# Performance work log

Hardware: AMD Instinct MI355X
Metric: run time of the kernel (lower is better)

Reference implementation:

```python
import jax, jax.numpy as jnp
import numpy as np

N, P, D, C = 2048, 64, 512, 32   # bs*n_vars, patch_num, hidden_dim, cluster_num
H, DFF, L = 8, 2048, 3           # heads, ffn dim, encoder layers
TEMP = 10.0
EPS = 1e-10
LN_EPS = 1e-5


def setup_inputs() -> dict:
    key = jax.random.key(0)
    ks = jax.random.split(key, 18)
    s = 0.02  # small init to keep activations sane
    inp = {}
    inp["input_series"] = jax.random.normal(ks[0], (N, P, D), jnp.float32)
    pi = jax.random.uniform(ks[1], (C,), jnp.float32) + 0.1
    inp["text_pi"] = pi / pi.sum()
    A = jax.random.uniform(ks[2], (C, C), jnp.float32) + 0.1
    inp["text_A"] = A / A.sum(axis=1, keepdims=True)
    # stacked per-layer TransformerEncoderLayer params (torch post-norm, relu)
    inp["qkv_w"] = jax.random.normal(ks[3], (L, 3 * D, D), jnp.float32) * s
    inp["qkv_b"] = jnp.zeros((L, 3 * D), jnp.float32)
    inp["out_w"] = jax.random.normal(ks[4], (L, D, D), jnp.float32) * s
    inp["out_b"] = jnp.zeros((L, D), jnp.float32)
    inp["ln1_w"] = jnp.ones((L, D), jnp.float32)
    inp["ln1_b"] = jnp.zeros((L, D), jnp.float32)
    inp["ff1_w"] = jax.random.normal(ks[5], (L, DFF, D), jnp.float32) * s
    inp["ff1_b"] = jnp.zeros((L, DFF), jnp.float32)
    inp["ff2_w"] = jax.random.normal(ks[6], (L, D, DFF), jnp.float32) * s
    inp["ff2_b"] = jnp.zeros((L, D), jnp.float32)
    inp["ln2_w"] = jnp.ones((L, D), jnp.float32)
    inp["ln2_b"] = jnp.zeros((L, D), jnp.float32)
    inp["mus"] = jax.random.normal(ks[7], (C, D), jnp.float32)
    return inp


def _layer_norm(x, w, b):
    m = x.mean(axis=-1, keepdims=True)
    v = ((x - m) ** 2).mean(axis=-1, keepdims=True)
    return (x - m) * jax.lax.rsqrt(v + LN_EPS) * w + b


def _encoder_layer(x, qkv_w, qkv_b, out_w, out_b, ln1_w, ln1_b,
                   ff1_w, ff1_b, ff2_w, ff2_b, ln2_w, ln2_b):
    n, p, d = x.shape
    dh = d // H
    qkv = x @ qkv_w.T + qkv_b                       # [n,p,3d]
    q, k, v = jnp.split(qkv, 3, axis=-1)
    def split_heads(t):
        return t.reshape(n, p, H, dh).transpose(0, 2, 1, 3)  # [n,h,p,dh]
    q, k, v = split_heads(q), split_heads(k), split_heads(v)
    scores = jnp.einsum('nhqd,nhkd->nhqk', q, k) / (dh ** 0.5)
    attn = jax.nn.softmax(scores, axis=-1)
    o = jnp.einsum('nhqk,nhkd->nhqd', attn, v)
    o = o.transpose(0, 2, 1, 3).reshape(n, p, d)
    o = o @ out_w.T + out_b
    x = _layer_norm(x + o, ln1_w, ln1_b)            # post-norm
    f = jax.nn.relu(x @ ff1_w.T + ff1_b) @ ff2_w.T + ff2_b
    return _layer_norm(x + f, ln2_w, ln2_b)


def reference(input_series, text_pi, text_A, qkv_w, qkv_b, out_w, out_b,
              ln1_w, ln1_b, ff1_w, ff1_b, ff2_w, ff2_b, ln2_w, ln2_b, mus):
    x = input_series
    for l in range(L):
        x = _encoder_layer(x, qkv_w[l], qkv_b[l], out_w[l], out_b[l],
                           ln1_w[l], ln1_b[l], ff1_w[l], ff1_b[l],
                           ff2_w[l], ff2_b[l], ln2_w[l], ln2_b[l])
    emb_ts = x                                       # [N,P,D]
    # ClusterCenters: softmax of exp(-||x - tanh(mu)||^2 / T)
    mu = jnp.tanh(mus)                               # [C,D]
    dist = ((emb_ts ** 2).sum(-1)[..., None]
            + (mu ** 2).sum(-1)[None, None, :]
            - 2.0 * jnp.einsum('npd,cd->npc', emb_ts, mu))  # [N,P,C]
    z = jnp.exp(-dist / TEMP)
    logits_all = z / z.sum(axis=-1, keepdims=True)
    log_za = jnp.log(logits_all + EPS)               # [N,P,C]
    # sequential HMM-style recursion over patches
    l0 = jax.nn.softmax(jnp.log(text_pi + EPS)[None, :] + log_za[:, 0], axis=-1)
    def step(c, lz):
        c2 = jax.nn.softmax(jnp.log(c @ text_A + EPS) + lz, axis=-1)
        return c2, c2
    _, ys = jax.lax.scan(step, l0, jnp.swapaxes(log_za[:, 1:], 0, 1))  # [P-1,N,C]
    cluster_probs = jnp.concatenate([l0[:, None], jnp.swapaxes(ys, 0, 1)], axis=1)
    entropy_loss = -jnp.sum(cluster_probs * jnp.log(cluster_probs + EPS), axis=-1).mean()
    return (cluster_probs, emb_ts, text_pi, text_A, entropy_loss)
```

## Files before the change

kernel.cpp:

```cpp
#include <hip/hip_runtime.h>
#include <stdint.h>


typedef __bf16 bf16;
typedef __bf16 bf16x2 __attribute__((ext_vector_type(2)));
typedef __bf16 bf16x4 __attribute__((ext_vector_type(4)));
typedef __bf16 bf16x8 __attribute__((ext_vector_type(8)));
typedef float  f32x4  __attribute__((ext_vector_type(4)));
typedef float  f32x2  __attribute__((ext_vector_type(2)));

#define EPSF 1e-10f
#define NROWS 131072L

__device__ __forceinline__ float bflo(uint32_t u){ return __uint_as_float(u << 16); }
__device__ __forceinline__ float bfhi(uint32_t u){ return __uint_as_float(u & 0xffff0000u); }

__device__ __forceinline__ void gload_lds16(const bf16* g, bf16* l){
  __builtin_amdgcn_global_load_lds((const __attribute__((address_space(1))) uint32_t*)g,
                                   (__attribute__((address_space(3))) uint32_t*)l,
                                   16, 0, 0);
}

__global__ void k_f2bf(const float* __restrict__ in, bf16* __restrict__ out, long n){
  const long stride = (long)gridDim.x * blockDim.x * 4;
  for (long i = ((long)blockIdx.x * blockDim.x + threadIdx.x) * 4; i < n; i += stride){
    f32x4 v = *(const f32x4*)(in + i);
    bf16x4 o = { (bf16)v[0], (bf16)v[1], (bf16)v[2], (bf16)v[3] };
    *(bf16x4*)(out + i) = o;
  }
}


#define MFMA_PH(RH, CH)                                                       \
  {                                                                           \
    __builtin_amdgcn_s_setprio(1);                                            \
    _Pragma("unroll")                                                         \
    for (int i2 = 0; i2 < 4; i2++) {                                          \
      _Pragma("unroll")                                                       \
      for (int j2 = 0; j2 < 2; j2++) {                                        \
        acc[(RH)*4+i2][(CH)*2+j2] = __builtin_amdgcn_mfma_f32_16x16x32_bf16(  \
            a[i2][0], b[CH][j2][0], acc[(RH)*4+i2][(CH)*2+j2], 0, 0, 0);      \
        acc[(RH)*4+i2][(CH)*2+j2] = __builtin_amdgcn_mfma_f32_16x16x32_bf16(  \
            a[i2][1], b[CH][j2][1], acc[(RH)*4+i2][(CH)*2+j2], 0, 0, 0);      \
      }                                                                       \
    }                                                                         \
    __builtin_amdgcn_s_setprio(0);                                            \
  }

#define RD_A(RH)                                                              \
  _Pragma("unroll")                                                           \
  for (int i2 = 0; i2 < 4; i2++) {                                            \
    a[i2][0] = *(const bf16x8*)&Ac[(aRow + (RH)*64 + i2*16) * 64 + sl0];      \
    a[i2][1] = *(const bf16x8*)&Ac[(aRow + (RH)*64 + i2*16) * 64 + sl1];      \
  }

#define RD_B(CH)                                                              \
  _Pragma("unroll")                                                           \
  for (int j2 = 0; j2 < 2; j2++) {                                            \
    b[CH][j2][0] = *(const bf16x8*)&Bc[(bRow + (CH)*32 + j2*16) * 64 + sl0];  \
    b[CH][j2][1] = *(const bf16x8*)&Bc[(bRow + (CH)*32 + j2*16) * 64 + sl1];  \
  }

#define ISSUE_A(dst, BI, KK) \
  gload_lds16(gA + (long)(BI)*64*lda + (KK), (dst) + (BI)*4096 + wslice)
#define ISSUE_B(dst, BI, KK) \
  gload_lds16(gB + (long)(BI)*64*K   + (KK), (dst) + (BI)*4096 + wslice)

#define WAITV(N)  asm volatile("s_waitcnt vmcnt(" #N ")" ::: "memory")
#define WAITL0    asm volatile("s_waitcnt lgkmcnt(0)" ::: "memory")
#define BARRIER   { __builtin_amdgcn_s_barrier(); asm volatile("" ::: "memory"); }

template<int RELU>
__global__ __launch_bounds__(512, 2)
void gemm256(const bf16* __restrict__ A, long lda,
             const bf16* __restrict__ W,
             const float* __restrict__ bias,
             bf16* __restrict__ Cb, long K, int nbx)
{
  const int tid  = threadIdx.x;
  const int wid  = tid >> 6;
  const int lane = tid & 63;
  const int wr = wid >> 2, wc = wid & 3;
  const long ldc = (long)nbx * 256;

  const unsigned nwg = gridDim.x;
  const unsigned q   = nwg >> 3;
  const unsigned swz = (blockIdx.x & 7) * q + (blockIdx.x >> 3);
  const unsigned bx  = swz % (unsigned)nbx;
  const unsigned by  = swz / (unsigned)nbx;
  const long bm = (long)by * 256;
  const long bn = (long)bx * 256;

  __shared__ __align__(16) bf16 smem[65536];
  bf16* const As0 = smem;
  bf16* const Bs0 = smem + 16384;
  bf16* const As1 = smem + 32768;
  bf16* const Bs1 = smem + 49152;

  const int srow   = wid * 8 + (lane >> 3);
  const int scol   = ((lane & 7) ^ ((lane >> 3) & 7)) * 8;
  const int wslice = wid * 512;
  const bf16* gA = A + (bm + srow) * lda + scol;
  const bf16* gB = W + (bn + srow) * K   + scol;

  const int fr = lane & 15, fg = lane >> 4;
  const int aRow = wr * 128 + fr;
  const int bRow = wc * 64  + fr;
  const int sl0 = ((0 + fg) ^ (fr & 7)) * 8;
  const int sl1 = ((4 + fg) ^ (fr & 7)) * 8;

  f32x4 acc[8][4];
#pragma unroll
  for (int i = 0; i < 8; i++)
#pragma unroll
    for (int j = 0; j < 4; j++) acc[i][j] = (f32x4){0.f, 0.f, 0.f, 0.f};

  bf16x8 a[4][2];
  bf16x8 b[2][2][2];

  const int nt = (int)(K >> 6);

  ISSUE_A(As0, 0, 0); ISSUE_A(As0, 2, 0);
  ISSUE_B(Bs0, 0, 0); ISSUE_B(Bs0, 1, 0);
  ISSUE_B(Bs0, 2, 0); ISSUE_B(Bs0, 3, 0);
  ISSUE_A(As0, 1, 0); ISSUE_A(As0, 3, 0);
  WAITV(2);
  BARRIER;

  for (int t = 0; t < nt; t++){
    bf16* const Ac = (t & 1) ? As1 : As0;
    bf16* const Bc = (t & 1) ? Bs1 : Bs0;
    bf16* const An = (t & 1) ? As0 : As1;
    bf16* const Bn = (t & 1) ? Bs0 : Bs1;
    const bool stage = (t + 1 < nt);
    const long kn = (long)(t + 1) << 6;

    RD_A(0); RD_B(0);
    if (stage){ ISSUE_A(An, 0, kn); ISSUE_A(An, 2, kn);
                ISSUE_B(Bn, 0, kn); ISSUE_B(Bn, 1, kn); }
    BARRIER;
    WAITL0;
    MFMA_PH(0, 0);
    BARRIER;

    RD_B(1);
    if (stage){ ISSUE_B(Bn, 2, kn); ISSUE_B(Bn, 3, kn); WAITV(6); }
    else      { WAITV(0); }
    BARRIER;
    WAITL0;
    MFMA_PH(0, 1);
    BARRIER;

    RD_A(1);
    if (stage){ ISSUE_A(An, 1, kn); ISSUE_A(An, 3, kn); }
    BARRIER;
    WAITL0;
    MFMA_PH(1, 0);
    BARRIER;

    WAITV(2);
    BARRIER;
    MFMA_PH(1, 1);
    BARRIER;
  }

  float* const cw = (float*)smem + wid * 2176;
  const long strip_row0 = bm + wr * 128;
  const long strip_col0 = bn + wc * 64;
  float bv[4];
#pragma unroll
  for (int j = 0; j < 4; j++) bv[j] = bias[strip_col0 + j * 16 + fr];
  const int rrow = lane >> 3;
  const int rcol = (lane & 7) * 8;

#pragma unroll
  for (int ch = 0; ch < 4; ch++){
#pragma unroll
    for (int i2 = 0; i2 < 2; i2++){
      const int i = ch * 2 + i2;
#pragma unroll
      for (int j = 0; j < 4; j++){
#pragma unroll
        for (int r = 0; r < 4; r++){
          float v = acc[i][j][r] + bv[j];
          if (RELU) v = fmaxf(v, 0.f);
          cw[(i2 * 16 + fg * 4 + r) * 68 + j * 16 + fr] = v;
        }
      }
    }
    WAITL0;
#pragma unroll
    for (int p = 0; p < 4; p++){
      const int row = p * 8 + rrow;
      f32x4 v0 = *(const f32x4*)&cw[row * 68 + rcol];
      f32x4 v1 = *(const f32x4*)&cw[row * 68 + rcol + 4];
      bf16x8 o = { (bf16)v0[0], (bf16)v0[1], (bf16)v0[2], (bf16)v0[3],
                   (bf16)v1[0], (bf16)v1[1], (bf16)v1[2], (bf16)v1[3] };
      *(bf16x8*)&Cb[(strip_row0 + ch * 32 + row) * ldc + strip_col0 + rcol] = o;
    }
    WAITL0;
  }
}

__global__ __launch_bounds__(256)
void attention(bf16* __restrict__ qkv)
{
  const int blk = blockIdx.x;
  const long n = blk >> 3;
  const int h  = blk & 7;
  const int tid = threadIdx.x;
  const int wid = tid >> 6, lane = tid & 63;

  __shared__ __align__(16) bf16 Qs[64][72];
  __shared__ __align__(16) bf16 Ks[64][72];
  __shared__ __align__(16) bf16 Vt[64][72];

  bf16* base = qkv + n * 64 * 1536 + h * 64;

  for (int c = tid; c < 512; c += 256){
    const int row = c >> 3, col = (c & 7) * 8;
    const long go = (long)row * 1536 + col;
    *(bf16x8*)&Qs[row][col] = *(const bf16x8*)(base + go);
    *(bf16x8*)&Ks[row][col] = *(const bf16x8*)(base + 512 + go);
    bf16x8 v = *(const bf16x8*)(base + 1024 + go);
#pragma unroll
    for (int e = 0; e < 8; e++) Vt[col + e][row] = v[e];
  }
  __syncthreads();

  const int fr = lane & 15, fg = lane >> 4;
  f32x4 sacc[4];
#pragma unroll
  for (int j = 0; j < 4; j++) sacc[j] = (f32x4){0.f, 0.f, 0.f, 0.f};
#pragma unroll
  for (int ks = 0; ks < 2; ks++){
    bf16x8 aa = *(const bf16x8*)&Qs[wid * 16 + fr][ks * 32 + fg * 8];
#pragma unroll
    for (int j = 0; j < 4; j++){
      bf16x8 bb = *(const bf16x8*)&Ks[j * 16 + fr][ks * 32 + fg * 8];
      sacc[j] = __builtin_amdgcn_mfma_f32_16x16x32_bf16(aa, bb, sacc[j], 0, 0, 0);
    }
  }

  float pv[4][4];
#pragma unroll
  for (int r = 0; r < 4; r++){
    float m = -1e30f;
#pragma unroll
    for (int j = 0; j < 4; j++) m = fmaxf(m, sacc[j][r]);
#pragma unroll
    for (int msk = 1; msk < 16; msk <<= 1) m = fmaxf(m, __shfl_xor(m, msk));
    float s = 0.f;
#pragma unroll
    for (int j = 0; j < 4; j++){
      float p = __expf((sacc[j][r] - m) * 0.125f);
      pv[j][r] = p; s += p;
    }
#pragma unroll
    for (int msk = 1; msk < 16; msk <<= 1) s += __shfl_xor(s, msk);
    const float inv = 1.f / s;
#pragma unroll
    for (int j = 0; j < 4; j++) pv[j][r] *= inv;
  }

#pragma unroll
  for (int j = 0; j < 4; j++)
#pragma unroll
    for (int r = 0; r < 4; r++)
      Qs[wid * 16 + fg * 4 + r][j * 16 + fr] = (bf16)pv[j][r];
  __syncthreads();

  f32x4 oacc[4];
#pragma unroll
  for (int j = 0; j < 4; j++) oacc[j] = (f32x4){0.f, 0.f, 0.f, 0.f};
#pragma unroll
  for (int ks = 0; ks < 2; ks++){
    bf16x8 aa = *(const bf16x8*)&Qs[wid * 16 + fr][ks * 32 + fg * 8];
#pragma unroll
    for (int j = 0; j < 4; j++){
      bf16x8 bb = *(const bf16x8*)&Vt[j * 16 + fr][ks * 32 + fg * 8];
      oacc[j] = __builtin_amdgcn_mfma_f32_16x16x32_bf16(aa, bb, oacc[j], 0, 0, 0);
    }
  }
#pragma unroll
  for (int j = 0; j < 4; j++)
#pragma unroll
    for (int r = 0; r < 4; r++)
      base[(long)(wid * 16 + fg * 4 + r) * 1536 + j * 16 + fr] = (bf16)oacc[j][r];
}

__global__ __launch_bounds__(256)
void resid_ln(const bf16* __restrict__ X, const bf16* __restrict__ O,
              const float* __restrict__ w, const float* __restrict__ b,
              bf16* __restrict__ Y, float* __restrict__ EF)
{
  const int wid = threadIdx.x >> 6, lane = threadIdx.x & 63;
  const long row = (long)blockIdx.x * 4 + wid;
  const uint4 xu = ((const uint4*)(X + row * 512))[lane];
  const uint4 ou = ((const uint4*)(O + row * 512))[lane];
  float s[8];
  s[0] = bflo(xu.x) + bflo(ou.x);  s[1] = bfhi(xu.x) + bfhi(ou.x);
  s[2] = bflo(xu.y) + bflo(ou.y);  s[3] = bfhi(xu.y) + bfhi(ou.y);
  s[4] = bflo(xu.z) + bflo(ou.z);  s[5] = bfhi(xu.z) + bfhi(ou.z);
  s[6] = bflo(xu.w) + bflo(ou.w);  s[7] = bfhi(xu.w) + bfhi(ou.w);
  float sum = 0.f, sq = 0.f;
#pragma unroll
  for (int e = 0; e < 8; e++){ sum += s[e]; sq += s[e] * s[e]; }
#pragma unroll
  for (int m = 1; m < 64; m <<= 1){ sum += __shfl_xor(sum, m); sq += __shfl_xor(sq, m); }
  const float mean = sum * (1.f / 512.f);
  const float var  = sq * (1.f / 512.f) - mean * mean;
  const float rs   = rsqrtf(var + 1e-5f);
  const f32x4 w0 = *(const f32x4*)(w + 8 * lane);
  const f32x4 w1 = *(const f32x4*)(w + 8 * lane + 4);
  const f32x4 b0 = *(const f32x4*)(b + 8 * lane);
  const f32x4 b1 = *(const f32x4*)(b + 8 * lane + 4);
  float o[8];
#pragma unroll
  for (int e = 0; e < 4; e++) o[e]     = (s[e]     - mean) * rs * w0[e] + b0[e];
#pragma unroll
  for (int e = 0; e < 4; e++) o[e + 4] = (s[e + 4] - mean) * rs * w1[e] + b1[e];
  bf16x8 ov = { (bf16)o[0], (bf16)o[1], (bf16)o[2], (bf16)o[3],
                (bf16)o[4], (bf16)o[5], (bf16)o[6], (bf16)o[7] };
  *(bf16x8*)(Y + row * 512 + 8 * lane) = ov;
  if (EF){
    f32x4 e0 = { o[0], o[1], o[2], o[3] };
    f32x4 e1 = { o[4], o[5], o[6], o[7] };
    *(f32x4*)(EF + row * 512 + 8 * lane) = e0;
    *(f32x4*)(EF + row * 512 + 8 * lane + 4) = e1;
  }
}

__global__ __launch_bounds__(256)
void k_mu(const float* __restrict__ mus, bf16* __restrict__ mubf, float* __restrict__ munorm)
{
  const int c = blockIdx.x, tid = threadIdx.x, lane = tid & 63, wid = tid >> 6;
  const f32x2 v = *(const f32x2*)(mus + c * 512 + 2 * tid);
  const float t0 = tanhf(v[0]), t1 = tanhf(v[1]);
  bf16x2 o2 = { (bf16)t0, (bf16)t1 };
  *(bf16x2*)(mubf + c * 512 + 2 * tid) = o2;
  float sq = t0 * t0 + t1 * t1;
#pragma unroll
  for (int m = 1; m < 64; m <<= 1) sq += __shfl_xor(sq, m);
  __shared__ float red[4];
  if (lane == 0) red[wid] = sq;
  __syncthreads();
  if (tid == 0) munorm[c] = red[0] + red[1] + red[2] + red[3];
}

__global__ __launch_bounds__(256)
void cluster_logza(const bf16* __restrict__ X, const bf16* __restrict__ MU,
                   const float* __restrict__ munorm, float* __restrict__ out)
{
  const int tid = threadIdx.x, lane = tid & 63, wid = tid >> 6;
  __shared__ __align__(16) bf16 mus[32][512];
  __shared__ float xs[512];
  __shared__ float red[4];
  __shared__ float dots[32];
  for (int c = tid; c < 2048; c += 256){
    const int r = c >> 6, col = (c & 63) * 8;
    *(bf16x8*)&mus[r][col] = *(const bf16x8*)(MU + r * 512 + col);
  }
  const int cc = tid >> 3, seg = tid & 7;
  const long row0 = (long)blockIdx.x * 16;
  __syncthreads();
  for (int rr = 0; rr < 16; rr++){
    const long row = row0 + rr;
    const uint32_t u = ((const uint32_t*)(X + row * 512))[tid];
    const float aa = bflo(u), bb = bfhi(u);
    xs[2 * tid] = aa; xs[2 * tid + 1] = bb;
    float sq = aa * aa + bb * bb;
#pragma unroll
    for (int m = 1; m < 64; m <<= 1) sq += __shfl_xor(sq, m);
    if (lane == 0) red[wid] = sq;
    __syncthreads();
    const float xn = red[0] + red[1] + red[2] + red[3];
    float p = 0.f;
#pragma unroll
    for (int jj = 0; jj < 8; jj++){
      const int col = jj * 64 + seg * 8;
      bf16x8 m8 = *(const bf16x8*)&mus[cc][col];
      const float* xv = &xs[col];
#pragma unroll
      for (int e = 0; e < 8; e++) p += xv[e] * (float)m8[e];
    }
#pragma unroll
    for (int m = 1; m < 8; m <<= 1) p += __shfl_xor(p, m);
    if (seg == 0) dots[cc] = p;
    __syncthreads();
    if (tid < 32){
      const float dist = xn + munorm[tid] - 2.f * dots[tid];
      const float lg = -dist * 0.1f;
      float mx = lg;
#pragma unroll
      for (int m = 1; m < 32; m <<= 1) mx = fmaxf(mx, __shfl_xor(mx, m, 32));
      const float z = __expf(lg - mx);
      float s = z;
#pragma unroll
      for (int m = 1; m < 32; m <<= 1) s += __shfl_xor(s, m, 32);
      out[row * 32 + tid] = logf(z / s + EPSF);
    }
    __syncthreads();
  }
}

__global__ __launch_bounds__(256)
void k_hmm(const float* __restrict__ lza, const float* __restrict__ pi,
           const float* __restrict__ A, float* __restrict__ cp, float* __restrict__ ent)
{
  __shared__ float As[32][33];
  const int tid = threadIdx.x;
  for (int i = tid; i < 1024; i += 256) As[i >> 5][i & 31] = A[i];
  __syncthreads();
  const int j = tid & 31;
  const long n = (long)blockIdx.x * 8 + (tid >> 5);
  const float* lz = lza + n * 2048;

  float c = logf(pi[j] + EPSF) + lz[j];
  {
    float mx = c;
#pragma unroll
    for (int m = 1; m < 32; m <<= 1) mx = fmaxf(mx, __shfl_xor(mx, m, 32));
    float z = __expf(c - mx), s = z;
#pragma unroll
    for (int m = 1; m < 32; m <<= 1) s += __shfl_xor(s, m, 32);
    c = z / s;
  }
  cp[n * 2048 + j] = c;
  float ea = -c * logf(c + EPSF);

  for (int p = 1; p < 64; p++){
    float y = 0.f;
#pragma unroll
    for (int i = 0; i < 32; i++) y += __shfl(c, i, 32) * As[i][j];
    float t = logf(y + EPSF) + lz[p * 32 + j];
    float mx = t;
#pragma unroll
    for (int m = 1; m < 32; m <<= 1) mx = fmaxf(mx, __shfl_xor(mx, m, 32));
    float z = __expf(t - mx), s = z;
#pragma unroll
    for (int m = 1; m < 32; m <<= 1) s += __shfl_xor(s, m, 32);
    c = z / s;
    cp[n * 2048 + p * 32 + j] = c;
    ea += -c * logf(c + EPSF);
  }
#pragma unroll
  for (int m = 1; m < 32; m <<= 1) ea += __shfl_xor(ea, m, 32);
  if (j == 0) atomicAdd(ent, ea * (1.f / 131072.f));
}

extern "C" void kernel_launch(void* const* d_in, const int* in_sizes, int n_in,
                              void* d_out, int out_size, void* d_ws, size_t ws_size,
                              hipStream_t stream)
{
  (void)in_sizes; (void)n_in; (void)out_size; (void)ws_size;
  const float* in_series = (const float*)d_in[0];
  const float* pi    = (const float*)d_in[1];
  const float* Amat  = (const float*)d_in[2];
  const float* qkv_w = (const float*)d_in[3];
  const float* qkv_b = (const float*)d_in[4];
  const float* out_w = (const float*)d_in[5];
  const float* out_b = (const float*)d_in[6];
  const float* ln1_w = (const float*)d_in[7];
  const float* ln1_b = (const float*)d_in[8];
  const float* ff1_w = (const float*)d_in[9];
  const float* ff1_b = (const float*)d_in[10];
  const float* ff2_w = (const float*)d_in[11];
  const float* ff2_b = (const float*)d_in[12];
  const float* ln2_w = (const float*)d_in[13];
  const float* ln2_b = (const float*)d_in[14];
  const float* mus   = (const float*)d_in[15];

  char* ws = (char*)d_ws;
  bf16* region0 = (bf16*)(ws);
  bf16* xb      = (bf16*)(ws + 536870912L);
  bf16* oproj   = (bf16*)(ws + 671088640L);
  bf16* w_qkv   = (bf16*)(ws + 805306368L);
  bf16* w_out   = (bf16*)(ws + 810024960L);
  bf16* w_ff1   = (bf16*)(ws + 811597824L);
  bf16* w_ff2   = (bf16*)(ws + 817889280L);
  bf16* mubf    = (bf16*)(ws + 824180736L);
  float* munorm = (float*)(ws + 824213504L);
  float* logza  = (float*)(ws);

  float* out_f = (float*)d_out;
  float* cp    = out_f;
  float* emb   = out_f + 4194304L;
  float* o_pi  = out_f + 71303168L;
  float* o_A   = out_f + 71303200L;
  float* o_ent = out_f + 71304224L;

  k_f2bf<<<8192, 256, 0, stream>>>(in_series, xb, 67108864L);
  k_f2bf<<<1024, 256, 0, stream>>>(qkv_w, w_qkv, 2359296L);
  k_f2bf<<<1024, 256, 0, stream>>>(out_w, w_out, 786432L);
  k_f2bf<<<1024, 256, 0, stream>>>(ff1_w, w_ff1, 3145728L);
  k_f2bf<<<1024, 256, 0, stream>>>(ff2_w, w_ff2, 3145728L);
  k_mu<<<32, 256, 0, stream>>>(mus, mubf, munorm);

  for (int l = 0; l < 3; l++){
    gemm256<0><<<3072, 512, 0, stream>>>(xb, 512, w_qkv + (long)l * 786432L,
                                         qkv_b + (long)l * 1536, region0, 512, 6);
    attention<<<16384, 256, 0, stream>>>(region0);
    gemm256<0><<<1024, 512, 0, stream>>>(region0, 1536, w_out + (long)l * 262144L,
                                         out_b + (long)l * 512, oproj, 512, 2);
    resid_ln<<<32768, 256, 0, stream>>>(xb, oproj, ln1_w + (long)l * 512,
                                        ln1_b + (long)l * 512, xb, nullptr);
    gemm256<1><<<4096, 512, 0, stream>>>(xb, 512, w_ff1 + (long)l * 1048576L,
                                         ff1_b + (long)l * 2048, region0, 512, 8);
    gemm256<0><<<1024, 512, 0, stream>>>(region0, 2048, w_ff2 + (long)l * 1048576L,
                                         ff2_b + (long)l * 512, oproj, 2048, 2);
    resid_ln<<<32768, 256, 0, stream>>>(xb, oproj, ln2_w + (long)l * 512,
                                        ln2_b + (long)l * 512, xb,
                                        (l == 2) ? emb : nullptr);
  }

  cluster_logza<<<8192, 256, 0, stream>>>(xb, mubf, munorm, logza);
  hipMemsetAsync(o_ent, 0, 4, stream);
  k_hmm<<<256, 256, 0, stream>>>(logza, pi, Amat, cp, o_ent);
  hipMemcpyAsync(o_pi, pi, 32 * sizeof(float), hipMemcpyDeviceToDevice, stream);
  hipMemcpyAsync(o_A, Amat, 1024 * sizeof(float), hipMemcpyDeviceToDevice, stream);
}
```

Baseline: 4.031 ms.

## Restructure GEMM main loop into two half-phases with fewer barriers and bf16 epilogue staging

The 256-tile GEMM main loop is reorganized from four MFMA phases, each bracketed by barriers, into two half-phases. All of B is read from LDS up front and the MFMAs are ordered by k-slice across the full column set. This cuts the barriers per K-tile from eight to two and reorders global-to-LDS prefetches so B is issued first. The epilogue now converts to bf16 before the LDS staging write, halving the staging bytes and replacing per-element conversion on read with plain bf16x8 loads. Holding all of B in registers raises VGPR pressure, and fewer barriers loosen the overlap between prefetch and compute.

```diff
diff --git a/kernel.cpp b/kernel.cpp
--- a/kernel.cpp
+++ b/kernel.cpp
@@ -31,17 +31,18 @@
 }
 
 
-#define MFMA_PH(RH, CH)                                                       \
+#define MFMA_HALF(RH)                                                         \
   {                                                                           \
     __builtin_amdgcn_s_setprio(1);                                            \
     _Pragma("unroll")                                                         \
-    for (int i2 = 0; i2 < 4; i2++) {                                          \
+    for (int kk = 0; kk < 2; kk++) {                                          \
       _Pragma("unroll")                                                       \
-      for (int j2 = 0; j2 < 2; j2++) {                                        \
-        acc[(RH)*4+i2][(CH)*2+j2] = __builtin_amdgcn_mfma_f32_16x16x32_bf16(  \
-            a[i2][0], b[CH][j2][0], acc[(RH)*4+i2][(CH)*2+j2], 0, 0, 0);      \
-        acc[(RH)*4+i2][(CH)*2+j2] = __builtin_amdgcn_mfma_f32_16x16x32_bf16(  \
-            a[i2][1], b[CH][j2][1], acc[(RH)*4+i2][(CH)*2+j2], 0, 0, 0);      \
+      for (int i2 = 0; i2 < 4; i2++) {                                        \
+        _Pragma("unroll")                                                     \
+        for (int jj = 0; jj < 4; jj++) {                                      \
+          acc[(RH)*4+i2][jj] = __builtin_amdgcn_mfma_f32_16x16x32_bf16(       \
+              a[i2][kk], b[jj][kk], acc[(RH)*4+i2][jj], 0, 0, 0);             \
+        }                                                                     \
       }                                                                       \
     }                                                                         \
     __builtin_amdgcn_s_setprio(0);                                            \
@@ -54,11 +55,11 @@
     a[i2][1] = *(const bf16x8*)&Ac[(aRow + (RH)*64 + i2*16) * 64 + sl1];      \
   }
 
-#define RD_B(CH)                                                              \
+#define RD_B_ALL                                                              \
   _Pragma("unroll")                                                           \
-  for (int j2 = 0; j2 < 2; j2++) {                                            \
-    b[CH][j2][0] = *(const bf16x8*)&Bc[(bRow + (CH)*32 + j2*16) * 64 + sl0];  \
-    b[CH][j2][1] = *(const bf16x8*)&Bc[(bRow + (CH)*32 + j2*16) * 64 + sl1];  \
+  for (int jj = 0; jj < 4; jj++) {                                            \
+    b[jj][0] = *(const bf16x8*)&Bc[(bRow + jj*16) * 64 + sl0];                \
+    b[jj][1] = *(const bf16x8*)&Bc[(bRow + jj*16) * 64 + sl1];                \
   }
 
 #define ISSUE_A(dst, BI, KK) \
@@ -116,13 +117,12 @@
     for (int j = 0; j < 4; j++) acc[i][j] = (f32x4){0.f, 0.f, 0.f, 0.f};
 
   bf16x8 a[4][2];
-  bf16x8 b[2][2][2];
+  bf16x8 b[4][2];
 
   const int nt = (int)(K >> 6);
 
+  ISSUE_B(Bs0, 0, 0); ISSUE_B(Bs0, 1, 0); ISSUE_B(Bs0, 2, 0); ISSUE_B(Bs0, 3, 0);
   ISSUE_A(As0, 0, 0); ISSUE_A(As0, 2, 0);
-  ISSUE_B(Bs0, 0, 0); ISSUE_B(Bs0, 1, 0);
-  ISSUE_B(Bs0, 2, 0); ISSUE_B(Bs0, 3, 0);
   ISSUE_A(As0, 1, 0); ISSUE_A(As0, 3, 0);
   WAITV(2);
   BARRIER;
@@ -135,36 +135,24 @@
     const bool stage = (t + 1 < nt);
     const long kn = (long)(t + 1) << 6;
 
-    RD_A(0); RD_B(0);
-    if (stage){ ISSUE_A(An, 0, kn); ISSUE_A(An, 2, kn);
-                ISSUE_B(Bn, 0, kn); ISSUE_B(Bn, 1, kn); }
-    BARRIER;
+    RD_A(0); RD_B_ALL;
+    if (stage){ ISSUE_B(Bn, 0, kn); ISSUE_B(Bn, 1, kn);
+                ISSUE_B(Bn, 2, kn); ISSUE_B(Bn, 3, kn);
+                ISSUE_A(An, 0, kn); ISSUE_A(An, 2, kn); }
     WAITL0;
-    MFMA_PH(0, 0);
-    BARRIER;
-
-    RD_B(1);
-    if (stage){ ISSUE_B(Bn, 2, kn); ISSUE_B(Bn, 3, kn); WAITV(6); }
-    else      { WAITV(0); }
-    BARRIER;
-    WAITL0;
-    MFMA_PH(0, 1);
+    MFMA_HALF(0);
+    if (stage){ WAITV(6); } else { WAITV(0); }
     BARRIER;
 
     RD_A(1);
     if (stage){ ISSUE_A(An, 1, kn); ISSUE_A(An, 3, kn); }
+    WAITL0;
+    MFMA_HALF(1);
+    if (stage){ WAITV(2); }
     BARRIER;
-    WAITL0;
-    MFMA_PH(1, 0);
-    BARRIER;
-
-    WAITV(2);
-    BARRIER;
-    MFMA_PH(1, 1);
-    BARRIER;
-  }
-
-  float* const cw = (float*)smem + wid * 2176;
+  }
+
+  bf16* const cw = smem + wid * 2304;
   const long strip_row0 = bm + wr * 128;
   const long strip_col0 = bn + wc * 64;
   float bv[4];
@@ -184,7 +172,7 @@
         for (int r = 0; r < 4; r++){
           float v = acc[i][j][r] + bv[j];
           if (RELU) v = fmaxf(v, 0.f);
-          cw[(i2 * 16 + fg * 4 + r) * 68 + j * 16 + fr] = v;
+          cw[(i2 * 16 + fg * 4 + r) * 72 + j * 16 + fr] = (bf16)v;
         }
       }
     }
@@ -192,10 +180,7 @@
 #pragma unroll
     for (int p = 0; p < 4; p++){
       const int row = p * 8 + rrow;
-      f32x4 v0 = *(const f32x4*)&cw[row * 68 + rcol];
-      f32x4 v1 = *(const f32x4*)&cw[row * 68 + rcol + 4];
-      bf16x8 o = { (bf16)v0[0], (bf16)v0[1], (bf16)v0[2], (bf16)v0[3],
-                   (bf16)v1[0], (bf16)v1[1], (bf16)v1[2], (bf16)v1[3] };
+      bf16x8 o = *(const bf16x8*)&cw[row * 72 + rcol];
       *(bf16x8*)&Cb[(strip_row0 + ch * 32 + row) * ldc + strip_col0 + rcol] = o;
     }
     WAITL0;
```

Measured after the change: 3.963 ms. No clear change (-1.7%).

## Restructure GEMM pipeline with deeper prefetch and quadrant-split warp tiles

Applied to the files above, without the earlier changes.

Reworks the 256x256 bf16 GEMM main loop. Each warp's tile becomes four 64x32 sub-tiles spread across the block's quadrants, so the first half of the next tile can be loaded into the buffer just consumed, two k-steps ahead. Several barriers between the LDS read and MFMA phases are removed, and the MFMA order is changed to iterate k innermost-outer. The epilogue now converts to bf16 before staging in a smaller LDS buffer. The intent is more load/compute overlap and fewer syncs, at the risk of subtle hazards from writing into the active buffer.

```diff
diff --git a/kernel.cpp b/kernel.cpp
--- a/kernel.cpp
+++ b/kernel.cpp
@@ -31,40 +31,41 @@
 }
 
 
-#define MFMA_PH(RH, CH)                                                       \
+#define MFMA_PH(SM, SN)                                                       \
   {                                                                           \
     __builtin_amdgcn_s_setprio(1);                                            \
     _Pragma("unroll")                                                         \
-    for (int i2 = 0; i2 < 4; i2++) {                                          \
+    for (int kk = 0; kk < 2; kk++) {                                          \
       _Pragma("unroll")                                                       \
-      for (int j2 = 0; j2 < 2; j2++) {                                        \
-        acc[(RH)*4+i2][(CH)*2+j2] = __builtin_amdgcn_mfma_f32_16x16x32_bf16(  \
-            a[i2][0], b[CH][j2][0], acc[(RH)*4+i2][(CH)*2+j2], 0, 0, 0);      \
-        acc[(RH)*4+i2][(CH)*2+j2] = __builtin_amdgcn_mfma_f32_16x16x32_bf16(  \
-            a[i2][1], b[CH][j2][1], acc[(RH)*4+i2][(CH)*2+j2], 0, 0, 0);      \
+      for (int i2 = 0; i2 < 4; i2++) {                                        \
+        _Pragma("unroll")                                                     \
+        for (int j2 = 0; j2 < 2; j2++) {                                      \
+          acc[(SM)*4+i2][(SN)*2+j2] = __builtin_amdgcn_mfma_f32_16x16x32_bf16(\
+              a[i2][kk], b[SN][j2][kk], acc[(SM)*4+i2][(SN)*2+j2], 0, 0, 0);  \
+        }                                                                     \
       }                                                                       \
     }                                                                         \
     __builtin_amdgcn_s_setprio(0);                                            \
   }
 
-#define RD_A(RH)                                                              \
+#define RD_A(SM)                                                              \
   _Pragma("unroll")                                                           \
   for (int i2 = 0; i2 < 4; i2++) {                                            \
-    a[i2][0] = *(const bf16x8*)&Ac[(aRow + (RH)*64 + i2*16) * 64 + sl0];      \
-    a[i2][1] = *(const bf16x8*)&Ac[(aRow + (RH)*64 + i2*16) * 64 + sl1];      \
-  }
-
-#define RD_B(CH)                                                              \
+    a[i2][0] = *(const bf16x8*)&Ac[(SM)*8192 + aBase + i2*1024 + sl0];        \
+    a[i2][1] = *(const bf16x8*)&Ac[(SM)*8192 + aBase + i2*1024 + sl1];        \
+  }
+
+#define RD_B(SN)                                                              \
   _Pragma("unroll")                                                           \
   for (int j2 = 0; j2 < 2; j2++) {                                            \
-    b[CH][j2][0] = *(const bf16x8*)&Bc[(bRow + (CH)*32 + j2*16) * 64 + sl0];  \
-    b[CH][j2][1] = *(const bf16x8*)&Bc[(bRow + (CH)*32 + j2*16) * 64 + sl1];  \
-  }
-
-#define ISSUE_A(dst, BI, KK) \
-  gload_lds16(gA + (long)(BI)*64*lda + (KK), (dst) + (BI)*4096 + wslice)
-#define ISSUE_B(dst, BI, KK) \
-  gload_lds16(gB + (long)(BI)*64*K   + (KK), (dst) + (BI)*4096 + wslice)
+    b[SN][j2][0] = *(const bf16x8*)&Bc[(SN)*8192 + bBase + j2*1024 + sl0];    \
+    b[SN][j2][1] = *(const bf16x8*)&Bc[(SN)*8192 + bBase + j2*1024 + sl1];    \
+  }
+
+#define ISSUE_A(dst, RO, KK) \
+  gload_lds16(gA + (long)(RO)*lda + (KK), (dst) + (RO)*64 + wsl)
+#define ISSUE_B(dst, RO, KK) \
+  gload_lds16(gB + (long)(RO)*K   + (KK), (dst) + (RO)*64 + wsl)
 
 #define WAITV(N)  asm volatile("s_waitcnt vmcnt(" #N ")" ::: "memory")
 #define WAITL0    asm volatile("s_waitcnt lgkmcnt(0)" ::: "memory")
@@ -97,15 +98,14 @@
   bf16* const As1 = smem + 32768;
   bf16* const Bs1 = smem + 49152;
 
-  const int srow   = wid * 8 + (lane >> 3);
-  const int scol   = ((lane & 7) ^ ((lane >> 3) & 7)) * 8;
-  const int wslice = wid * 512;
-  const bf16* gA = A + (bm + srow) * lda + scol;
-  const bf16* gB = W + (bn + srow) * K   + scol;
+  const int gswz = ((lane & 7) ^ ((lane >> 3) & 7)) * 8;
+  const int wsl  = wid * 512;
+  const bf16* gA = A + (bm + wid * 8 + (lane >> 3)) * lda + gswz;
+  const bf16* gB = W + (bn + wid * 8 + (lane >> 3)) * K   + gswz;
 
   const int fr = lane & 15, fg = lane >> 4;
-  const int aRow = wr * 128 + fr;
-  const int bRow = wc * 64  + fr;
+  const int aBase = (wr * 64 + fr) * 64;
+  const int bBase = (wc * 32 + fr) * 64;
   const int sl0 = ((0 + fg) ^ (fr & 7)) * 8;
   const int sl1 = ((4 + fg) ^ (fr & 7)) * 8;
 
@@ -120,11 +120,15 @@
 
   const int nt = (int)(K >> 6);
 
-  ISSUE_A(As0, 0, 0); ISSUE_A(As0, 2, 0);
-  ISSUE_B(Bs0, 0, 0); ISSUE_B(Bs0, 1, 0);
-  ISSUE_B(Bs0, 2, 0); ISSUE_B(Bs0, 3, 0);
-  ISSUE_A(As0, 1, 0); ISSUE_A(As0, 3, 0);
-  WAITV(2);
+  ISSUE_A(As0, 0, 0);   ISSUE_A(As0, 64, 0);
+  ISSUE_B(Bs0, 0, 0);   ISSUE_B(Bs0, 64, 0);
+  ISSUE_A(As0, 128, 0); ISSUE_A(As0, 192, 0);
+  ISSUE_B(Bs0, 128, 0); ISSUE_B(Bs0, 192, 0);
+  if (nt > 1){
+    ISSUE_A(As1, 0, 64); ISSUE_A(As1, 64, 64);
+    ISSUE_B(Bs1, 0, 64); ISSUE_B(Bs1, 64, 64);
+  }
+  WAITV(8);
   BARRIER;
 
   for (int t = 0; t < nt; t++){
@@ -132,73 +136,76 @@
     bf16* const Bc = (t & 1) ? Bs1 : Bs0;
     bf16* const An = (t & 1) ? As0 : As1;
     bf16* const Bn = (t & 1) ? Bs0 : Bs1;
-    const bool stage = (t + 1 < nt);
-    const long kn = (long)(t + 1) << 6;
+    const bool s1 = (t + 1 < nt);
+    const bool s2 = (t + 2 < nt);
+    const long kn  = (long)(t + 1) << 6;
+    const long kn2 = (long)(t + 2) << 6;
 
     RD_A(0); RD_B(0);
-    if (stage){ ISSUE_A(An, 0, kn); ISSUE_A(An, 2, kn);
-                ISSUE_B(Bn, 0, kn); ISSUE_B(Bn, 1, kn); }
-    BARRIER;
+    if (s1){ ISSUE_A(An, 128, kn); ISSUE_A(An, 192, kn); }
     WAITL0;
     MFMA_PH(0, 0);
+    if (s1){ WAITV(6); } else { WAITV(0); }
     BARRIER;
 
     RD_B(1);
-    if (stage){ ISSUE_B(Bn, 2, kn); ISSUE_B(Bn, 3, kn); WAITV(6); }
-    else      { WAITV(0); }
-    BARRIER;
+    if (s1){ ISSUE_B(Bn, 128, kn); ISSUE_B(Bn, 192, kn); }
     WAITL0;
     MFMA_PH(0, 1);
     BARRIER;
 
     RD_A(1);
-    if (stage){ ISSUE_A(An, 1, kn); ISSUE_A(An, 3, kn); }
-    BARRIER;
+    if (s2){ ISSUE_A(Ac, 0, kn2); ISSUE_A(Ac, 64, kn2); }
     WAITL0;
     MFMA_PH(1, 0);
     BARRIER;
 
-    WAITV(2);
+    if (s2){ ISSUE_B(Bc, 0, kn2); ISSUE_B(Bc, 64, kn2); }
+    MFMA_PH(1, 1);
+    if (s2)      { WAITV(8); }
+    else if (s1) { WAITV(4); }
     BARRIER;
-    MFMA_PH(1, 1);
-    BARRIER;
-  }
-
-  float* const cw = (float*)smem + wid * 2176;
-  const long strip_row0 = bm + wr * 128;
-  const long strip_col0 = bn + wc * 64;
+  }
+
+  bf16* const cw = smem + wid * 1280;
   float bv[4];
 #pragma unroll
-  for (int j = 0; j < 4; j++) bv[j] = bias[strip_col0 + j * 16 + fr];
-  const int rrow = lane >> 3;
-  const int rcol = (lane & 7) * 8;
-
-#pragma unroll
-  for (int ch = 0; ch < 4; ch++){
-#pragma unroll
-    for (int i2 = 0; i2 < 2; i2++){
-      const int i = ch * 2 + i2;
-#pragma unroll
-      for (int j = 0; j < 4; j++){
-#pragma unroll
-        for (int r = 0; r < 4; r++){
-          float v = acc[i][j][r] + bv[j];
-          if (RELU) v = fmaxf(v, 0.f);
-          cw[(i2 * 16 + fg * 4 + r) * 68 + j * 16 + fr] = v;
+  for (int sn = 0; sn < 2; sn++)
+#pragma unroll
+    for (int j2 = 0; j2 < 2; j2++)
+      bv[sn * 2 + j2] = bias[bn + sn * 128 + wc * 32 + j2 * 16 + fr];
+
+#pragma unroll
+  for (int sm = 0; sm < 2; sm++){
+#pragma unroll
+    for (int sn = 0; sn < 2; sn++){
+#pragma unroll
+      for (int ch = 0; ch < 2; ch++){
+#pragma unroll
+        for (int i2 = 0; i2 < 2; i2++){
+#pragma unroll
+          for (int j2 = 0; j2 < 2; j2++){
+#pragma unroll
+            for (int r = 0; r < 4; r++){
+              float v = acc[sm * 4 + ch * 2 + i2][sn * 2 + j2][r] + bv[sn * 2 + j2];
+              if (RELU) v = fmaxf(v, 0.f);
+              cw[(i2 * 16 + fg * 4 + r) * 40 + j2 * 16 + fr] = (bf16)v;
+            }
+          }
         }
+        WAITL0;
+        const long r0 = bm + sm * 128 + wr * 64 + ch * 32;
+        const long c0 = bn + sn * 128 + wc * 32;
+#pragma unroll
+        for (int p = 0; p < 2; p++){
+          const int row = p * 16 + (lane >> 2);
+          const int colg = (lane & 3) * 8;
+          bf16x8 o = *(const bf16x8*)&cw[row * 40 + colg];
+          *(bf16x8*)&Cb[(r0 + row) * ldc + c0 + colg] = o;
+        }
+        WAITL0;
       }
     }
-    WAITL0;
-#pragma unroll
-    for (int p = 0; p < 4; p++){
-      const int row = p * 8 + rrow;
-      f32x4 v0 = *(const f32x4*)&cw[row * 68 + rcol];
-      f32x4 v1 = *(const f32x4*)&cw[row * 68 + rcol + 4];
-      bf16x8 o = { (bf16)v0[0], (bf16)v0[1], (bf16)v0[2], (bf16)v0[3],
-                   (bf16)v1[0], (bf16)v1[1], (bf16)v1[2], (bf16)v1[3] };
-      *(bf16x8*)&Cb[(strip_row0 + ch * 32 + row) * ldc + strip_col0 + rcol] = o;
-    }
-    WAITL0;
   }
 }
 
```

New measurement: 3.934 ms. -2.4%, faster.
